# Optimization experiments

Measured on AMD Instinct MI355X. Metric: run time of the kernel, lower is better.

The kernel has to match this reference:

```python
import jax, jax.numpy as jnp
import numpy as np

B, T = 32, 128
D, H, HD = 512, 8, 64
FF, E, N = 2048, 8, 3
NF = 16            # Fourier features
VOCAB, FEAT = 119, 200
SCALE = 10.0
EPS = 1e-5


def layernorm(x, g, b):
    m = jnp.mean(x, axis=-1, keepdims=True)
    v = jnp.mean((x - m) ** 2, axis=-1, keepdims=True)
    return (x - m) * jax.lax.rsqrt(v + EPS) * g + b


def setup_inputs() -> dict:
    key = jax.random.key(0)
    ks = jax.random.split(key, 32)
    f32 = jnp.float32
    inp = {
        "src": jax.random.randint(ks[0], (B, T), 0, VOCAB),
        "frac": jax.random.uniform(ks[1], (B, T), dtype=f32),
        "embed_table": jax.random.normal(ks[2], (VOCAB, FEAT), f32),
        "W_m2v": jax.random.normal(ks[3], (FEAT, D), f32) * 0.05,
        "b_m2v": jnp.zeros((D,), f32),
        "pb_W": jax.random.normal(ks[4], (1, NF), f32) * 0.1,
        "pb_b": jax.random.uniform(ks[5], (NF,), f32) * 2 * np.pi,
        "pb_a": jax.random.normal(ks[6], (NF,), f32),
        "Wk": jax.random.normal(ks[7], (N, D, D), f32) * 0.03,
        "bk": jnp.zeros((N, D), f32),
        "Wv": jax.random.normal(ks[8], (N, D, D), f32) * 0.03,
        "bv": jnp.zeros((N, D), f32),
        "Wo": jax.random.normal(ks[9], (N, D, D), f32) * 0.03,
        "bo": jnp.zeros((N, D), f32),
        "ln1_g": jnp.ones((N, D), f32),
        "ln1_b": jnp.zeros((N, D), f32),
        "ln2_g": jnp.ones((N, D), f32),
        "ln2_b": jnp.zeros((N, D), f32),
        "gate_W": jax.random.normal(ks[10], (N, D, E), f32) * 0.05,
        "gate_b": jnp.zeros((N, E), f32),
        "eW1": jax.random.normal(ks[11], (N, E, D, FF), f32) * 0.03,
        "eb1": jnp.zeros((N, E, FF), f32),
        "eW2": jax.random.normal(ks[12], (N, E, FF, D), f32) * 0.02,
        "eb2": jnp.zeros((N, E, D), f32),
    }
    return inp


def reference(src, frac, embed_table, W_m2v, b_m2v, pb_W, pb_b, pb_a,
              Wk, bk, Wv, bv, Wo, bo, ln1_g, ln1_b, ln2_g, ln2_b,
              gate_W, gate_b, eW1, eb1, eW2, eb2):
    # Embedder: mat2vec lookup + linear projection
    x = embed_table[src] @ W_m2v + b_m2v                      # [B,T,D]

    # Fourier positional bias: pb[b,i,j] = cos((frac_j - frac_i)*scale * W + b) @ a
    diffs = (frac[:, None, :] - frac[:, :, None]) * SCALE     # [B,T,T]
    rff = jnp.cos(diffs[..., None] * pb_W[0] + pb_b)          # [B,T,T,NF]
    pb = rff @ pb_a                                           # [B,T,T]

    for i in range(N):
        # --- Fourier-bias attention ---
        K = (x @ Wk[i] + bk[i]).reshape(B, T, H, HD).transpose(0, 2, 1, 3)  # [B,H,T,HD]
        V = (x @ Wv[i] + bv[i]).reshape(B, T, H, HD).transpose(0, 2, 1, 3)
        # scores[b,h,i,j,d] = K[b,h,j,d] + pb[b,i,j]; weighted = sum_j scores*V
        # factor: sum_j K*V (indep of i) + sum_j pb[b,i,j]*V[b,h,j,d]
        kv = jnp.sum(K * V, axis=2)                           # [B,H,HD]
        pbv = jnp.einsum('bij,bhjd->bhid', pb, V)             # [B,H,T,HD]
        wv = (pbv + kv[:, :, None, :]).transpose(0, 2, 1, 3).reshape(B, T, D)
        x = layernorm(x + wv @ Wo[i] + bo[i], ln1_g[i], ln1_b[i])

        # --- MoE FFN, top-2 gating (eval mode: no dropout/noise) ---
        probs = jax.nn.softmax(x @ gate_W[i] + gate_b[i], axis=-1)   # [B,T,E]
        top2_s, top2_e = jax.lax.top_k(probs, 2)                     # [B,T,2]
        w = jnp.sum(jax.nn.one_hot(top2_e, E, dtype=x.dtype) * top2_s[..., None], axis=2)  # [B,T,E]
        h = jax.nn.relu(jnp.einsum('btd,edf->btef', x, eW1[i]) + eb1[i])  # [B,T,E,FF]
        eo = jnp.einsum('btef,efd->bted', h, eW2[i]) + eb2[i]             # [B,T,E,D]
        ff = jnp.einsum('bte,bted->btd', w, eo)
        x = layernorm(x + ff, ln2_g[i], ln2_b[i])
    return x
```

## Files before the change

### kernel.cpp

```cpp
#include <hip/hip_runtime.h>
#include <math.h>

#define B_    32
#define T_    128
#define D_    512
#define FF_   2048
#define E_    8
#define NL_   3
#define NF_   16
#define FEAT_ 200
#define BT_   4096

typedef short bf16x8 __attribute__((ext_vector_type(8)));
typedef float f32x4  __attribute__((ext_vector_type(4)));

__device__ inline unsigned short f2bf(float f) {
    unsigned u = __float_as_uint(f);
    unsigned r = (u + 0x7fffu + ((u >> 16) & 1u)) >> 16;
    return (unsigned short)r;
}
__device__ inline void split_bf(float f, unsigned short& h, unsigned short& l) {
    h = f2bf(f);
    float fh = __uint_as_float(((unsigned)h) << 16);
    l = f2bf(f - fh);
}

__device__ __forceinline__ void ld_g2l(const unsigned short* g, unsigned short* l)
{
    __builtin_amdgcn_global_load_lds(
        (const __attribute__((address_space(1))) unsigned int*)(uintptr_t)g,
        (__attribute__((address_space(3))) unsigned int*)(uintptr_t)l,
        16, 0, 0);
}

template <int MODE, bool SPLITOUT, bool RELU>
__global__ __launch_bounds__(256)
void mgemm_k(const unsigned short* __restrict__ Ah, const unsigned short* __restrict__ Al,
             const unsigned short* __restrict__ Bh, const unsigned short* __restrict__ Bl,
             const float* __restrict__ bias,
             float* __restrict__ Cf, unsigned short* __restrict__ Ch,
             unsigned short* __restrict__ Cl,
             int M, int K, int N, long strB, int strBias,
             const int* __restrict__ counts, const int* __restrict__ offsets,
             const int* __restrict__ tok_list)
{
    const int z  = blockIdx.z;
    const int m0 = blockIdx.y * 128, n0 = blockIdx.x * 128;
    int rows, rowoff = 0;
    if constexpr (MODE != 0) {
        rows = counts[z];
        if (m0 >= rows) return;
        rowoff = offsets[z];
    } else {
        rows = M;
    }
    const unsigned short* Bhb = Bh + (long)z * strB;
    const unsigned short* Blb = Bl + (long)z * strB;
    const float* biasb = bias + (long)z * strBias;

    __shared__ unsigned short S[2][4 * 4096];

    const int tid  = threadIdx.x;
    const int w    = tid >> 6, lane = tid & 63;
    const int wm = w & 1, wn = w >> 1;
    const int l15 = lane & 15, quad = lane >> 4;

    const int lrow0 = w * 32 + (lane >> 2);
    const int lrow1 = lrow0 + 16;
    const int sseg  = (lane & 3) ^ ((lane >> 3) & 3);
    const int lb0   = (w * 2 + 0) * 512;
    const int lb1   = (w * 2 + 1) * 512;

    long ga0, ga1;
    if constexpr (MODE == 1) {
        int m_a = m0 + lrow0; if (m_a >= rows) m_a = rows - 1;
        int m_b = m0 + lrow1; if (m_b >= rows) m_b = rows - 1;
        ga0 = tok_list[z * BT_ + m_a];
        ga1 = tok_list[z * BT_ + m_b];
    } else if constexpr (MODE == 2) {
        int m_a = m0 + lrow0; if (m_a >= rows) m_a = rows - 1;
        int m_b = m0 + lrow1; if (m_b >= rows) m_b = rows - 1;
        ga0 = (long)rowoff + m_a;
        ga1 = (long)rowoff + m_b;
    } else {
        ga0 = m0 + lrow0;
        ga1 = m0 + lrow1;
    }
    const long aoff0 = ga0 * (long)K + sseg * 8;
    const long aoff1 = ga1 * (long)K + sseg * 8;
    const long boff0 = (long)(n0 + lrow0) * K + sseg * 8;
    const long boff1 = (long)(n0 + lrow1) * K + sseg * 8;

    f32x4 acc[4][4];
#pragma unroll
    for (int i = 0; i < 4; ++i)
#pragma unroll
        for (int j = 0; j < 4; ++j) acc[i][j] = (f32x4)0.f;

    const int xq = quad ^ ((l15 >> 1) & 3);

    {
        unsigned short* Sb = S[0];
        ld_g2l(Ah  + aoff0, Sb + 0 * 4096 + lb0);
        ld_g2l(Ah  + aoff1, Sb + 0 * 4096 + lb1);
        ld_g2l(Al  + aoff0, Sb + 1 * 4096 + lb0);
        ld_g2l(Al  + aoff1, Sb + 1 * 4096 + lb1);
        ld_g2l(Bhb + boff0, Sb + 2 * 4096 + lb0);
        ld_g2l(Bhb + boff1, Sb + 2 * 4096 + lb1);
        ld_g2l(Blb + boff0, Sb + 3 * 4096 + lb0);
        ld_g2l(Blb + boff1, Sb + 3 * 4096 + lb1);
    }

    unsigned short* Scur = S[0];
    unsigned short* Snxt = S[1];

    for (int k0 = 0; k0 < K; k0 += 32) {
        __syncthreads();

        if (k0 + 32 < K) {
            int kn = k0 + 32;
            ld_g2l(Ah  + aoff0 + kn, Snxt + 0 * 4096 + lb0);
            ld_g2l(Ah  + aoff1 + kn, Snxt + 0 * 4096 + lb1);
            ld_g2l(Al  + aoff0 + kn, Snxt + 1 * 4096 + lb0);
            ld_g2l(Al  + aoff1 + kn, Snxt + 1 * 4096 + lb1);
            ld_g2l(Bhb + boff0 + kn, Snxt + 2 * 4096 + lb0);
            ld_g2l(Bhb + boff1 + kn, Snxt + 2 * 4096 + lb1);
            ld_g2l(Blb + boff0 + kn, Snxt + 3 * 4096 + lb0);
            ld_g2l(Blb + boff1 + kn, Snxt + 3 * 4096 + lb1);
        }

        bf16x8 ah4[4], al4[4], bh4[4], bl4[4];
#pragma unroll
        for (int i = 0; i < 4; ++i) {
            int ro = (wm * 64 + i * 16 + l15) * 32 + xq * 8;
            ah4[i] = *(const bf16x8*)&Scur[0 * 4096 + ro];
            al4[i] = *(const bf16x8*)&Scur[1 * 4096 + ro];
        }
#pragma unroll
        for (int j = 0; j < 4; ++j) {
            int ro = (wn * 64 + j * 16 + l15) * 32 + xq * 8;
            bh4[j] = *(const bf16x8*)&Scur[2 * 4096 + ro];
            bl4[j] = *(const bf16x8*)&Scur[3 * 4096 + ro];
        }
#pragma unroll
        for (int i = 0; i < 4; ++i)
#pragma unroll
            for (int j = 0; j < 4; ++j) {
                acc[i][j] = __builtin_amdgcn_mfma_f32_16x16x32_bf16(al4[i], bh4[j], acc[i][j], 0, 0, 0);
                acc[i][j] = __builtin_amdgcn_mfma_f32_16x16x32_bf16(ah4[i], bl4[j], acc[i][j], 0, 0, 0);
                acc[i][j] = __builtin_amdgcn_mfma_f32_16x16x32_bf16(ah4[i], bh4[j], acc[i][j], 0, 0, 0);
            }

        unsigned short* t = Scur; Scur = Snxt; Snxt = t;
    }

#pragma unroll
    for (int i = 0; i < 4; ++i) {
#pragma unroll
        for (int r = 0; r < 4; ++r) {
            int gm = m0 + wm * 64 + i * 16 + quad * 4 + r;
            if (MODE != 0 && gm >= rows) continue;
            long crow = (MODE != 0) ? ((long)rowoff + gm) : (long)gm;
#pragma unroll
            for (int j = 0; j < 4; ++j) {
                int col = n0 + wn * 64 + j * 16 + l15;
                float v = acc[i][j][r] + biasb[col];
                if constexpr (RELU) v = fmaxf(v, 0.f);
                if constexpr (SPLITOUT) {
                    unsigned short h, l;
                    split_bf(v, h, l);
                    Ch[crow * (long)N + col] = h;
                    Cl[crow * (long)N + col] = l;
                } else {
                    Cf[crow * (long)N + col] = v;
                }
            }
        }
    }
}

template <bool WF32, bool SPLIT>
__global__ __launch_bounds__(256)
void gemm_k(const float* __restrict__ A, const float* __restrict__ Bm,
            const float* __restrict__ bias, float* __restrict__ C,
            unsigned short* __restrict__ Oh, unsigned short* __restrict__ Ol,
            int K, int lda, int ldb, int ldc,
            long strA, long strB, long strC, int strBias)
{
    const int z  = blockIdx.z;
    const int m0 = blockIdx.y * 64, n0 = blockIdx.x * 64;
    const float* Ab    = A    + (long)z * strA;
    const float* Bb    = Bm   + (long)z * strB;
    const float* biasb = bias + (long)z * strBias;

    __shared__ float As[16][68];
    __shared__ float Bs[16][64];

    const int tid = threadIdx.x;
    const int tx  = tid & 15, ty = tid >> 4;
    const int ar  = tid >> 2;
    const int akc = (tid & 3) * 4;
    const float* Arow = Ab + (long)(m0 + ar) * lda;
    const int bkr = tid >> 4;
    const int bnc = (tid & 15) * 4;

    float acc[4][4];
#pragma unroll
    for (int i = 0; i < 4; ++i)
#pragma unroll
        for (int j = 0; j < 4; ++j) acc[i][j] = 0.f;

    for (int k0 = 0; k0 < K; k0 += 16) {
        if (k0 + 16 <= K) {
            float4 a = *(const float4*)(Arow + k0 + akc);
            As[akc + 0][ar] = a.x; As[akc + 1][ar] = a.y;
            As[akc + 2][ar] = a.z; As[akc + 3][ar] = a.w;
        } else {
#pragma unroll
            for (int j = 0; j < 4; ++j) {
                int kk = k0 + akc + j;
                As[akc + j][ar] = (kk < K) ? Arow[kk] : 0.f;
            }
        }
        {
            int kk = k0 + bkr;
            float4 b;
            if (kk < K) b = *(const float4*)(Bb + (long)kk * ldb + n0 + bnc);
            else        b = make_float4(0.f, 0.f, 0.f, 0.f);
            *(float4*)&Bs[bkr][bnc] = b;
        }
        __syncthreads();
#pragma unroll
        for (int k = 0; k < 16; ++k) {
            float4 av = *(const float4*)&As[k][ty * 4];
            float4 bv = *(const float4*)&Bs[k][tx * 4];
            float am[4] = {av.x, av.y, av.z, av.w};
            float bn[4] = {bv.x, bv.y, bv.z, bv.w};
#pragma unroll
            for (int i = 0; i < 4; ++i)
#pragma unroll
                for (int j = 0; j < 4; ++j)
                    acc[i][j] = fmaf(am[i], bn[j], acc[i][j]);
        }
        __syncthreads();
    }
#pragma unroll
    for (int i = 0; i < 4; ++i) {
        long row = (long)z * (strC / 1) + 0;
        (void)row;
        long base = ((long)z * strC) + (long)(m0 + ty * 4 + i) * ldc + n0 + tx * 4;
        const float* bp = biasb + n0 + tx * 4;
#pragma unroll
        for (int j = 0; j < 4; ++j) {
            float v = acc[i][j] + bp[j];
            if constexpr (WF32) C[base + j] = v;
            if constexpr (SPLIT) {
                unsigned short h, l;
                split_bf(v, h, l);
                Oh[base + j] = h;
                Ol[base + j] = l;
            }
        }
    }
}

__global__ __launch_bounds__(256)
void transpose_split_k(const float* __restrict__ in,
                       unsigned short* __restrict__ oh, unsigned short* __restrict__ ol,
                       int R, int C, long strIn, long strOut)
{
    __shared__ float tile[32][33];
    const float* I = in + (long)blockIdx.z * strIn;
    unsigned short* OH = oh + (long)blockIdx.z * strOut;
    unsigned short* OL = ol + (long)blockIdx.z * strOut;
    int c0 = blockIdx.x * 32, r0 = blockIdx.y * 32;
    int tx = threadIdx.x & 31, ty = threadIdx.x >> 5;
#pragma unroll
    for (int i = 0; i < 4; ++i)
        tile[ty + i * 8][tx] = I[(long)(r0 + ty + i * 8) * C + c0 + tx];
    __syncthreads();
#pragma unroll
    for (int i = 0; i < 4; ++i) {
        unsigned short h, l;
        split_bf(tile[tx][ty + i * 8], h, l);
        long o = (long)(c0 + ty + i * 8) * R + r0 + tx;
        OH[o] = h; OL[o] = l;
    }
}

__global__ void bias_cat_k(const float* __restrict__ a, const float* __restrict__ b,
                           float* __restrict__ o)
{
    int i = blockIdx.x * 256 + threadIdx.x;
    o[i] = (i < D_) ? a[i] : b[i - D_];
}

__global__ void embed_gather_k(const int* __restrict__ src,
                               const float* __restrict__ table,
                               float* __restrict__ emb)
{
    int t = blockIdx.x;
    int v = src[t];
    for (int k = threadIdx.x; k < FEAT_; k += 256)
        emb[t * FEAT_ + k] = table[v * FEAT_ + k];
}

__global__ __launch_bounds__(256)
void pb_k(const float* __restrict__ frac, const float* __restrict__ pbW,
          const float* __restrict__ pbb, const float* __restrict__ pba,
          float* __restrict__ pb)
{
    int idx = blockIdx.x * 256 + threadIdx.x;
    int b = idx >> 14;
    int i = (idx >> 7) & 127;
    int j = idx & 127;
    float diff = (frac[b * T_ + j] - frac[b * T_ + i]) * 10.0f;
    float s = 0.f;
#pragma unroll
    for (int f = 0; f < NF_; ++f)
        s = fmaf(cosf(fmaf(diff, pbW[f], pbb[f])), pba[f], s);
    pb[idx] = s;
}

__global__ __launch_bounds__(256)
void kv_k(const float* __restrict__ KV, float* __restrict__ kv)
{
    int idx = blockIdx.x * 256 + threadIdx.x;
    int b = idx >> 9, c = idx & 511;
    const float* Kp = KV + (long)b * T_ * 1024 + c;
    float s = 0.f;
    for (int t = 0; t < T_; ++t) {
        const float* p = Kp + t * 1024;
        s = fmaf(p[0], p[D_], s);
    }
    kv[idx] = s;
}

__global__ __launch_bounds__(256)
void ln_res_k(const float* __restrict__ x, const float* __restrict__ add,
              const float* __restrict__ g, const float* __restrict__ b,
              float* __restrict__ out, unsigned short* __restrict__ oh,
              unsigned short* __restrict__ ol)
{
    int wave = threadIdx.x >> 6, lane = threadIdx.x & 63;
    int row = blockIdx.x * 4 + wave;
    const float* xr = x   + (long)row * D_ + lane * 8;
    const float* ar = add + (long)row * D_ + lane * 8;
    float v[8]; float s = 0.f;
#pragma unroll
    for (int j = 0; j < 8; ++j) { v[j] = xr[j] + ar[j]; s += v[j]; }
#pragma unroll
    for (int off = 32; off > 0; off >>= 1) s += __shfl_xor(s, off, 64);
    float mean = s * (1.f / D_);
    float q = 0.f;
#pragma unroll
    for (int j = 0; j < 8; ++j) { float d = v[j] - mean; q += d * d; }
#pragma unroll
    for (int off = 32; off > 0; off >>= 1) q += __shfl_xor(q, off, 64);
    float inv = rsqrtf(q * (1.f / D_) + 1e-5f);
    float* orow = out + (long)row * D_ + lane * 8;
    unsigned short* hrow = oh + (long)row * D_ + lane * 8;
    unsigned short* lrow = ol + (long)row * D_ + lane * 8;
#pragma unroll
    for (int j = 0; j < 8; ++j) {
        int c = lane * 8 + j;
        float o = (v[j] - mean) * inv * g[c] + b[c];
        orow[j] = o;
        unsigned short hh, ll;
        split_bf(o, hh, ll);
        hrow[j] = hh; lrow[j] = ll;
    }
}

__global__ __launch_bounds__(256)
void ln_moe_k(const float* __restrict__ x, const float* __restrict__ eo,
              const int* __restrict__ tok_slot, const float* __restrict__ tok_w,
              const int* __restrict__ offsets,
              const float* __restrict__ g, const float* __restrict__ b,
              float* __restrict__ out, unsigned short* __restrict__ oh,
              unsigned short* __restrict__ ol)
{
    int wave = threadIdx.x >> 6, lane = threadIdx.x & 63;
    int row = blockIdx.x * 4 + wave;
    int  c0 = tok_slot[row * 2], c1 = tok_slot[row * 2 + 1];
    float w0 = tok_w[row * 2],  w1 = tok_w[row * 2 + 1];
    long r0 = offsets[c0 >> 12] + (c0 & 4095);
    long r1 = offsets[c1 >> 12] + (c1 & 4095);
    const float* xr = x  + (long)row * D_ + lane * 8;
    const float* e0 = eo + r0 * D_ + lane * 8;
    const float* e1 = eo + r1 * D_ + lane * 8;
    float v[8]; float s = 0.f;
#pragma unroll
    for (int j = 0; j < 8; ++j) {
        v[j] = xr[j] + w0 * e0[j] + w1 * e1[j];
        s += v[j];
    }
#pragma unroll
    for (int off = 32; off > 0; off >>= 1) s += __shfl_xor(s, off, 64);
    float mean = s * (1.f / D_);
    float q = 0.f;
#pragma unroll
    for (int j = 0; j < 8; ++j) { float d = v[j] - mean; q += d * d; }
#pragma unroll
    for (int off = 32; off > 0; off >>= 1) q += __shfl_xor(q, off, 64);
    float inv = rsqrtf(q * (1.f / D_) + 1e-5f);
    float* orow = out + (long)row * D_ + lane * 8;
    unsigned short* hrow = oh + (long)row * D_ + lane * 8;
    unsigned short* lrow = ol + (long)row * D_ + lane * 8;
#pragma unroll
    for (int j = 0; j < 8; ++j) {
        int c = lane * 8 + j;
        float o = (v[j] - mean) * inv * g[c] + b[c];
        orow[j] = o;
        unsigned short hh, ll;
        split_bf(o, hh, ll);
        hrow[j] = hh; lrow[j] = ll;
    }
}

__global__ __launch_bounds__(256)
void gate_k(const float* __restrict__ x, const float* __restrict__ gW,
            const float* __restrict__ gb, int* __restrict__ counts,
            int* __restrict__ tok_list, int* __restrict__ tok_slot,
            float* __restrict__ tok_w)
{
    int wave = threadIdx.x >> 6, lane = threadIdx.x & 63;
    int t = blockIdx.x * 4 + wave;
    float acc[8];
#pragma unroll
    for (int e = 0; e < 8; ++e) acc[e] = 0.f;
    const float* xr = x + (long)t * D_;
#pragma unroll
    for (int j = 0; j < 8; ++j) {
        int d = lane * 8 + j;
        float xv = xr[d];
        const float* w = gW + d * 8;
#pragma unroll
        for (int e = 0; e < 8; ++e) acc[e] = fmaf(xv, w[e], acc[e]);
    }
#pragma unroll
    for (int off = 32; off > 0; off >>= 1)
#pragma unroll
        for (int e = 0; e < 8; ++e) acc[e] += __shfl_xor(acc[e], off, 64);

    if (lane == 0) {
        float m = -1e30f;
#pragma unroll
        for (int e = 0; e < 8; ++e) { acc[e] += gb[e]; m = fmaxf(m, acc[e]); }
        float p[8]; float s = 0.f;
#pragma unroll
        for (int e = 0; e < 8; ++e) { p[e] = expf(acc[e] - m); s += p[e]; }
        float inv = 1.f / s;
        int e1 = 0;
        for (int e = 1; e < 8; ++e) if (p[e] > p[e1]) e1 = e;
        int e2 = -1;
        for (int e = 0; e < 8; ++e) {
            if (e == e1) continue;
            if (e2 < 0 || p[e] > p[e2]) e2 = e;
        }
        int s1 = atomicAdd(&counts[e1], 1);
        tok_list[e1 * BT_ + s1] = t;
        tok_slot[t * 2]     = (e1 << 12) | s1;
        tok_w[t * 2]        = p[e1] * inv;
        int s2 = atomicAdd(&counts[e2], 1);
        tok_list[e2 * BT_ + s2] = t;
        tok_slot[t * 2 + 1] = (e2 << 12) | s2;
        tok_w[t * 2 + 1]    = p[e2] * inv;
    }
}

__global__ void zero_counts_k(int* __restrict__ counts)
{
    if (threadIdx.x < E_) counts[threadIdx.x] = 0;
}

__global__ void scan_k(const int* __restrict__ counts, int* __restrict__ offsets)
{
    if (threadIdx.x == 0) {
        int s = 0;
        for (int e = 0; e < E_; ++e) { offsets[e] = s; s += counts[e]; }
    }
}

extern "C" void kernel_launch(void* const* d_in, const int* in_sizes, int n_in,
                              void* d_out, int out_size, void* d_ws, size_t ws_size,
                              hipStream_t stream)
{
    const int*   src   = (const int*)  d_in[0];
    const float* frac  = (const float*)d_in[1];
    const float* table = (const float*)d_in[2];
    const float* W_m2v = (const float*)d_in[3];
    const float* b_m2v = (const float*)d_in[4];
    const float* pbW   = (const float*)d_in[5];
    const float* pbb   = (const float*)d_in[6];
    const float* pba   = (const float*)d_in[7];
    const float* Wk    = (const float*)d_in[8];
    const float* bk    = (const float*)d_in[9];
    const float* Wv    = (const float*)d_in[10];
    const float* bv    = (const float*)d_in[11];
    const float* Wo    = (const float*)d_in[12];
    const float* bo    = (const float*)d_in[13];
    const float* ln1g  = (const float*)d_in[14];
    const float* ln1b  = (const float*)d_in[15];
    const float* ln2g  = (const float*)d_in[16];
    const float* ln2b  = (const float*)d_in[17];
    const float* gW    = (const float*)d_in[18];
    const float* gb    = (const float*)d_in[19];
    const float* eW1   = (const float*)d_in[20];
    const float* eb1   = (const float*)d_in[21];
    const float* eW2   = (const float*)d_in[22];
    const float* eb2   = (const float*)d_in[23];

    float* ws   = (float*)d_ws;
    float* x    = ws;  ws += (long)BT_ * D_;
    float* pb   = ws;  ws += (long)B_ * T_ * T_;
    float* eo   = ws;  ws += (long)2 * BT_ * D_;
    float* kv   = ws;  ws += B_ * D_;
    float* tokw = ws;  ws += 2 * BT_;
    float* kvbias = ws; ws += 2 * D_;
    unsigned short* us = (unsigned short*)ws;
    unsigned short* x_h   = us;  us += (long)BT_ * D_;
    unsigned short* x_l   = us;  us += (long)BT_ * D_;
    unsigned short* Wkv_h = us;  us += (long)2 * D_ * D_;
    unsigned short* Wkv_l = us;  us += (long)2 * D_ * D_;
    unsigned short* Wo_h  = us;  us += (long)D_ * D_;
    unsigned short* Wo_l  = us;  us += (long)D_ * D_;
    unsigned short* e1_h  = us;  us += (long)E_ * FF_ * D_;
    unsigned short* e1_l  = us;  us += (long)E_ * FF_ * D_;
    unsigned short* e2_h  = us;  us += (long)E_ * D_ * FF_;
    unsigned short* e2_l  = us;  us += (long)E_ * D_ * FF_;
    int* counts  = (int*)us;
    int* offsets = counts + 8;
    int* toklist = offsets + 8;
    int* tokslot = toklist + E_ * BT_;
    char* ar = (char*)(tokslot + 2 * BT_);
    ar = (char*)(((size_t)ar + 255) & ~(size_t)255);
    unsigned short* h_h = (unsigned short*)ar;
    unsigned short* h_l = h_h + (long)2 * BT_ * FF_;
    float* emb  = (float*)ar;
    float* KVb  = emb + (long)BT_ * FEAT_;
    float* tmp  = KVb + (long)BT_ * 2 * D_;
    unsigned short* wv_h = (unsigned short*)(tmp + (long)BT_ * D_);
    unsigned short* wv_l = wv_h + (long)BT_ * D_;

    embed_gather_k<<<BT_, 256, 0, stream>>>(src, table, emb);
    gemm_k<true, true><<<dim3(8, 64, 1), 256, 0, stream>>>(
        emb, W_m2v, b_m2v, x, x_h, x_l, FEAT_, FEAT_, D_, D_, 0, 0, 0, 0);

    pb_k<<<(B_ * T_ * T_) / 256, 256, 0, stream>>>(frac, pbW, pbb, pba, pb);

    for (int i = 0; i < NL_; ++i) {
        transpose_split_k<<<dim3(16, 16, 1), 256, 0, stream>>>(
            Wk + (long)i * D_ * D_, Wkv_h, Wkv_l, D_, D_, 0, 0);
        transpose_split_k<<<dim3(16, 16, 1), 256, 0, stream>>>(
            Wv + (long)i * D_ * D_, Wkv_h + (long)D_ * D_, Wkv_l + (long)D_ * D_,
            D_, D_, 0, 0);
        transpose_split_k<<<dim3(16, 16, 1), 256, 0, stream>>>(
            Wo + (long)i * D_ * D_, Wo_h, Wo_l, D_, D_, 0, 0);
        transpose_split_k<<<dim3(64, 16, E_), 256, 0, stream>>>(
            eW1 + (long)i * E_ * D_ * FF_, e1_h, e1_l, D_, FF_,
            (long)D_ * FF_, (long)FF_ * D_);
        transpose_split_k<<<dim3(16, 64, E_), 256, 0, stream>>>(
            eW2 + (long)i * E_ * FF_ * D_, e2_h, e2_l, FF_, D_,
            (long)FF_ * D_, (long)D_ * FF_);
        bias_cat_k<<<4, 256, 0, stream>>>(bk + i * D_, bv + i * D_, kvbias);

        mgemm_k<0, false, false><<<dim3(8, 32, 1), 256, 0, stream>>>(
            x_h, x_l, Wkv_h, Wkv_l, kvbias,
            KVb, nullptr, nullptr, BT_, D_, 2 * D_, 0, 0,
            nullptr, nullptr, nullptr);

        kv_k<<<(B_ * D_) / 256, 256, 0, stream>>>(KVb, kv);

        gemm_k<false, true><<<dim3(8, 2, B_), 256, 0, stream>>>(
            pb, KVb + D_, kv, nullptr, wv_h, wv_l, T_, T_, 2 * D_, D_,
            (long)T_ * T_, (long)T_ * 2 * D_, (long)T_ * D_, D_);

        mgemm_k<0, false, false><<<dim3(4, 32, 1), 256, 0, stream>>>(
            wv_h, wv_l, Wo_h, Wo_l, bo + i * D_,
            tmp, nullptr, nullptr, BT_, D_, D_, 0, 0, nullptr, nullptr, nullptr);

        ln_res_k<<<BT_ / 4, 256, 0, stream>>>(x, tmp, ln1g + i * D_, ln1b + i * D_,
                                              x, x_h, x_l);

        zero_counts_k<<<1, 64, 0, stream>>>(counts);
        gate_k<<<BT_ / 4, 256, 0, stream>>>(x, gW + (long)i * D_ * E_, gb + i * E_,
                                            counts, toklist, tokslot, tokw);
        scan_k<<<1, 1, 0, stream>>>(counts, offsets);

        mgemm_k<1, true, true><<<dim3(16, 32, E_), 256, 0, stream>>>(
            x_h, x_l, e1_h, e1_l, eb1 + (long)i * E_ * FF_,
            nullptr, h_h, h_l, 0, D_, FF_,
            (long)FF_ * D_, FF_, counts, offsets, toklist);
        mgemm_k<2, false, false><<<dim3(4, 32, E_), 256, 0, stream>>>(
            h_h, h_l, e2_h, e2_l, eb2 + (long)i * E_ * D_,
            eo, nullptr, nullptr, 0, FF_, D_,
            (long)D_ * FF_, D_, counts, offsets, toklist);

        float* dst = (i == NL_ - 1) ? (float*)d_out : x;
        ln_moe_k<<<BT_ / 4, 256, 0, stream>>>(x, eo, tokslot, tokw, offsets,
                                              ln2g + i * D_, ln2b + i * D_,
                                              dst, x_h, x_l);
    }
}
```

Measured before the change: 1.342 ms.

## Aggregate MoE gate routing atomics per block via shared-memory counters

The gating kernel now processes 64 tokens per block instead of 4. It reorganizes the logit dot product so each lane owns one expert and one 64-wide chunk of D, with all lanes doing the softmax and top-2 redundantly. Expert slot counters are accumulated with shared-memory atomics, then one global atomicAdd per expert per block reserves a base, replacing two global atomics per token. This cuts global atomic contention but launches only 64 blocks, which may underuse the GPU for a kernel that is already small.

New measurement: 1.216 ms. 9.4% less time.

```diff
diff --git a/kernel.cpp b/kernel.cpp
--- a/kernel.cpp
+++ b/kernel.cpp
@@ -10,6 +10,9 @@
 #define NF_   16
 #define FEAT_ 200
 #define BT_   4096
+
+#define GB_   64
+#define TPB_  (BT_ / GB_)
 
 typedef short bf16x8 __attribute__((ext_vector_type(8)));
 typedef float f32x4  __attribute__((ext_vector_type(4)));
@@ -246,8 +249,6 @@
     }
 #pragma unroll
     for (int i = 0; i < 4; ++i) {
-        long row = (long)z * (strC / 1) + 0;
-        (void)row;
         long base = ((long)z * strC) + (long)(m0 + ty * 4 + i) * ldc + n0 + tx * 4;
         const float* bp = biasb + n0 + tx * 4;
 #pragma unroll
@@ -424,48 +425,85 @@
             int* __restrict__ tok_list, int* __restrict__ tok_slot,
             float* __restrict__ tok_w)
 {
-    int wave = threadIdx.x >> 6, lane = threadIdx.x & 63;
-    int t = blockIdx.x * 4 + wave;
-    float acc[8];
-#pragma unroll
-    for (int e = 0; e < 8; ++e) acc[e] = 0.f;
-    const float* xr = x + (long)t * D_;
-#pragma unroll
-    for (int j = 0; j < 8; ++j) {
-        int d = lane * 8 + j;
-        float xv = xr[d];
-        const float* w = gW + d * 8;
-#pragma unroll
-        for (int e = 0; e < 8; ++e) acc[e] = fmaf(xv, w[e], acc[e]);
-    }
-#pragma unroll
-    for (int off = 32; off > 0; off >>= 1)
-#pragma unroll
-        for (int e = 0; e < 8; ++e) acc[e] += __shfl_xor(acc[e], off, 64);
-
-    if (lane == 0) {
-        float m = -1e30f;
-#pragma unroll
-        for (int e = 0; e < 8; ++e) { acc[e] += gb[e]; m = fmaxf(m, acc[e]); }
+    __shared__ int scnt[E_];
+    __shared__ int sbase[E_];
+    __shared__ int sent[TPB_][2];
+
+    const int wave = threadIdx.x >> 6, lane = threadIdx.x & 63;
+    const int e  = lane & 7;
+    const int ch = lane >> 3;
+    const int t0 = blockIdx.x * TPB_;
+
+    if (threadIdx.x < E_) scnt[threadIdx.x] = 0;
+    __syncthreads();
+
+    for (int it = 0; it < TPB_ / 4; ++it) {
+        const int tl = it * 4 + wave;
+        const int t  = t0 + tl;
+
+        const float4* x4 = (const float4*)(x + (long)t * D_ + ch * 64);
+        const float*  wr = gW + (long)ch * 64 * E_ + e;
+        float acc = 0.f;
+#pragma unroll
+        for (int d4 = 0; d4 < 16; ++d4) {
+            float4 xv = x4[d4];
+            acc = fmaf(xv.x, wr[(d4 * 4 + 0) * 8], acc);
+            acc = fmaf(xv.y, wr[(d4 * 4 + 1) * 8], acc);
+            acc = fmaf(xv.z, wr[(d4 * 4 + 2) * 8], acc);
+            acc = fmaf(xv.w, wr[(d4 * 4 + 3) * 8], acc);
+        }
+        acc += __shfl_xor(acc, 8, 64);
+        acc += __shfl_xor(acc, 16, 64);
+        acc += __shfl_xor(acc, 32, 64);
+        acc += gb[e];
+
+        float lg[8];
+#pragma unroll
+        for (int ee = 0; ee < 8; ++ee)
+            lg[ee] = __shfl(acc, (lane & 56) | ee, 64);
+
+        float m = lg[0];
+#pragma unroll
+        for (int ee = 1; ee < 8; ++ee) m = fmaxf(m, lg[ee]);
         float p[8]; float s = 0.f;
 #pragma unroll
-        for (int e = 0; e < 8; ++e) { p[e] = expf(acc[e] - m); s += p[e]; }
+        for (int ee = 0; ee < 8; ++ee) { p[ee] = expf(lg[ee] - m); s += p[ee]; }
         float inv = 1.f / s;
         int e1 = 0;
-        for (int e = 1; e < 8; ++e) if (p[e] > p[e1]) e1 = e;
-        int e2 = -1;
-        for (int e = 0; e < 8; ++e) {
-            if (e == e1) continue;
-            if (e2 < 0 || p[e] > p[e2]) e2 = e;
-        }
-        int s1 = atomicAdd(&counts[e1], 1);
-        tok_list[e1 * BT_ + s1] = t;
-        tok_slot[t * 2]     = (e1 << 12) | s1;
-        tok_w[t * 2]        = p[e1] * inv;
-        int s2 = atomicAdd(&counts[e2], 1);
-        tok_list[e2 * BT_ + s2] = t;
-        tok_slot[t * 2 + 1] = (e2 << 12) | s2;
-        tok_w[t * 2 + 1]    = p[e2] * inv;
+#pragma unroll
+        for (int ee = 1; ee < 8; ++ee) if (p[ee] > p[e1]) e1 = ee;
+        int e2 = (e1 == 0) ? 1 : 0;
+#pragma unroll
+        for (int ee = 0; ee < 8; ++ee) {
+            if (ee == e1) continue;
+            if (p[ee] > p[e2]) e2 = ee;
+        }
+
+        if (lane == 0) {
+            int ls1 = atomicAdd(&scnt[e1], 1);
+            int ls2 = atomicAdd(&scnt[e2], 1);
+            sent[tl][0] = (e1 << 12) | ls1;
+            sent[tl][1] = (e2 << 12) | ls2;
+            tok_w[t * 2]     = p[e1] * inv;
+            tok_w[t * 2 + 1] = p[e2] * inv;
+        }
+    }
+    __syncthreads();
+
+    if (threadIdx.x < E_)
+        sbase[threadIdx.x] = atomicAdd(&counts[threadIdx.x], scnt[threadIdx.x]);
+    __syncthreads();
+
+    for (int tl = threadIdx.x; tl < TPB_; tl += 256) {
+        const int t = t0 + tl;
+#pragma unroll
+        for (int kk = 0; kk < 2; ++kk) {
+            int v    = sent[tl][kk];
+            int ee   = v >> 12;
+            int slot = sbase[ee] + (v & 4095);
+            tok_list[ee * BT_ + slot] = t;
+            tok_slot[t * 2 + kk] = (ee << 12) | slot;
+        }
     }
 }
 
@@ -584,8 +622,8 @@
                                               x, x_h, x_l);
 
         zero_counts_k<<<1, 64, 0, stream>>>(counts);
-        gate_k<<<BT_ / 4, 256, 0, stream>>>(x, gW + (long)i * D_ * E_, gb + i * E_,
-                                            counts, toklist, tokslot, tokw);
+        gate_k<<<GB_, 256, 0, stream>>>(x, gW + (long)i * D_ * E_, gb + i * E_,
+                                        counts, toklist, tokslot, tokw);
         scan_k<<<1, 1, 0, stream>>>(counts, offsets);
 
         mgemm_k<1, true, true><<<dim3(16, 32, E_), 256, 0, stream>>>(
```
